# Kernel optimization log

Hardware: AMD Instinct MI355X
Metric: run time of the kernel (lower is better)

The kernel has to match this reference:

```python
import jax, jax.numpy as jnp
import numpy as np

H, HK, D, WIN = 16, 4, 128, 1024  # n_head, n_kv_head, head_dim, left window


def rmsnorm(x):
    eps = jnp.asarray(jnp.finfo(x.dtype).eps, x.dtype)
    return x * jax.lax.rsqrt(jnp.mean(x * x, axis=-1, keepdims=True) + eps)


def rope(x, cos, sin):
    d = x.shape[-1] // 2
    x1, x2 = x[..., :d], x[..., d:]
    return jnp.concatenate([x1 * cos + x2 * sin, x1 * -sin + x2 * cos], axis=-1)


def setup_inputs() -> dict:
    key = jax.random.key(0)
    ks = jax.random.split(key, 12)
    B, T, C = 4, 2048, 2048
    t = jnp.arange(T, dtype=jnp.float32)[:, None]
    inv = 1.0 / (10000.0 ** (jnp.arange(D // 2, dtype=jnp.float32) / (D // 2)))
    ang = t * inv[None, :]  # [T, D/2]
    return {
        "x": jax.random.normal(ks[0], (B, T, C), jnp.float32),
        "x0": jax.random.normal(ks[1], (B, T, C), jnp.float32),
        "ve": jnp.zeros((B, T, C), jnp.float32),  # unused in add_init_qkv branch
        "cos": jnp.cos(ang)[None, :, None, :],  # [1,T,1,D/2]
        "sin": jnp.sin(ang)[None, :, None, :],
        "Wq": jax.random.normal(ks[2], (H * D, C), jnp.float32) * 0.02,
        "Wk": jax.random.normal(ks[3], (HK * D, C), jnp.float32) * 0.02,
        "Wv": jax.random.normal(ks[4], (HK * D, C), jnp.float32) * 0.02,
        "Wproj": jax.random.normal(ks[5], (C, H * D), jnp.float32) * 0.02,
        "alpha_q": jnp.ones((1,), jnp.float32),
        "beta_q": jax.random.uniform(ks[6], (1,), jnp.float32),
        "alpha_k": jnp.ones((1,), jnp.float32),
        "beta_k": jax.random.uniform(ks[7], (1,), jnp.float32),
        "alpha_v": jnp.ones((1,), jnp.float32),
        "beta_v": jax.random.uniform(ks[8], (1,), jnp.float32),
    }


def reference(x, x0, ve, cos, sin, Wq, Wk, Wv, Wproj,
              alpha_q, beta_q, alpha_k, beta_k, alpha_v, beta_v):
    B, T, C = x.shape
    g = H // HK  # GQA group size

    q = (x @ Wq.T).reshape(B, T, H, D)
    k = (x @ Wk.T).reshape(B, T, HK, D)
    v = (x @ Wv.T).reshape(B, T, HK, D)
    v_init = v

    # is_target + add_init_qkv + learn_init_coeffs: blend with projections of norm(x0)
    x0n = rmsnorm(x0)
    cqx = (x0n @ Wq.T).reshape(B, T, H, D)
    ckx = (x0n @ Wk.T).reshape(B, T, HK, D)
    cvx = (x0n @ Wv.T).reshape(B, T, HK, D)
    q = alpha_q * q + beta_q * cqx
    k = alpha_k * k + beta_k * ckx
    v = alpha_v * v + beta_v * cvx

    # rotary + qk-norm + 1.2 scale
    q = rmsnorm(rope(q, cos, sin)) * 1.2
    k = rmsnorm(rope(k, cos, sin)) * 1.2

    qg = q.reshape(B, T, HK, g, D)
    scale = 1.0 / np.sqrt(D)
    scores = jnp.einsum('bqhgd,bkhd->bhgqk', qg, k) * scale  # [B,HK,g,T,T]
    i = jnp.arange(T)[:, None]
    j = jnp.arange(T)[None, :]
    mask = (j <= i) & (i - j <= WIN)
    scores = jnp.where(mask, scores, -jnp.inf)
    p = jax.nn.softmax(scores, axis=-1)
    y = jnp.einsum('bhgqk,bkhd->bqhgd', p, v).reshape(B, T, H * D)

    y = y @ Wproj.T
    return (y, v_init)
```

## Files before the change

kernel.cpp:

```cpp
#include <hip/hip_runtime.h>
#include <hip/hip_bf16.h>
#include <math.h>


using bf16 = __hip_bfloat16;
typedef __attribute__((ext_vector_type(8))) short bf16x8;
typedef __attribute__((ext_vector_type(4))) short bf16x4;
typedef __attribute__((ext_vector_type(4))) float f32x4;

constexpr int Bb = 4, Ts = 2048, Cc = 2048, NH = 16, NKV = 4, Dh = 128, WIN = 1024;
constexpr float EPS = 1.1920929e-07f;

__device__ __forceinline__ void gld16(void* lds, const void* g) {
  __builtin_amdgcn_global_load_lds(
      (__attribute__((address_space(1))) unsigned int*)((void*)g),
      (__attribute__((address_space(3))) unsigned int*)lds, 16, 0, 0);
}

__device__ __forceinline__ unsigned short bfbits(float f) {
  bf16 h = __float2bfloat16(f);
  return __builtin_bit_cast(unsigned short, h);
}

__device__ __forceinline__ void store_out(float* p, float v) { *p = v; }
__device__ __forceinline__ void store_out(bf16* p, float v) { *p = __float2bfloat16(v); }

__device__ __forceinline__ f32x4 mfma16(bf16x4 a, bf16x4 b, f32x4 c) {
#if __has_builtin(__builtin_amdgcn_mfma_f32_16x16x16bf16_1k)
  return __builtin_amdgcn_mfma_f32_16x16x16bf16_1k(a, b, c, 0, 0, 0);
#else
  bf16x8 a8 = {a[0], a[1], a[2], a[3], 0, 0, 0, 0};
  bf16x8 b8 = {b[0], b[1], b[2], b[3], 0, 0, 0, 0};
  return __builtin_amdgcn_mfma_f32_16x16x32_bf16(a8, b8, c, 0, 0, 0);
#endif
}

__global__ __launch_bounds__(256) void convert_w4(
    const float* __restrict__ s0, bf16* __restrict__ d0,
    const float* __restrict__ s1, bf16* __restrict__ d1,
    const float* __restrict__ s2, bf16* __restrict__ d2,
    const float* __restrict__ s3, bf16* __restrict__ d3) {
  const int bid = blockIdx.x;
  const float* src;
  bf16* dst;
  int base;
  if (bid < 4096)      { src = s0; dst = d0; base = 0; }
  else if (bid < 5120) { src = s1; dst = d1; base = 4096; }
  else if (bid < 6144) { src = s2; dst = d2; base = 5120; }
  else                 { src = s3; dst = d3; base = 6144; }
  const int i = (bid - base) * 256 + threadIdx.x;
  float4 v = ((const float4*)src)[i];
  ushort4 u;
  u.x = bfbits(v.x); u.y = bfbits(v.y); u.z = bfbits(v.z); u.w = bfbits(v.w);
  ((ushort4*)dst)[i] = u;
}

__global__ __launch_bounds__(256) void prep(
    const float* __restrict__ x, const float* __restrict__ x0,
    const float* aq_p, const float* bq_p, const float* ak_p, const float* bk_p,
    bf16* __restrict__ xq, bf16* __restrict__ xk,
    bf16* __restrict__ xb, bf16* __restrict__ x0n) {
  const int row = blockIdx.x, tid = threadIdx.x;
  const float4* xr = (const float4*)(x + (size_t)row * Cc);
  const float4* nr = (const float4*)(x0 + (size_t)row * Cc);
  float4 xa[2], na[2];
  float ss = 0.f;
#pragma unroll
  for (int j = 0; j < 2; ++j) {
    xa[j] = xr[tid + j * 256];
    na[j] = nr[tid + j * 256];
    ss += na[j].x * na[j].x + na[j].y * na[j].y + na[j].z * na[j].z + na[j].w * na[j].w;
  }
#pragma unroll
  for (int o = 32; o; o >>= 1) ss += __shfl_xor(ss, o);
  __shared__ float red[4];
  if ((tid & 63) == 0) red[tid >> 6] = ss;
  __syncthreads();
  const float rms = rsqrtf((red[0] + red[1] + red[2] + red[3]) * (1.f / Cc) + EPS);
  const float aq = *aq_p, bq = *bq_p, ak = *ak_p, bk = *bk_p;
#pragma unroll
  for (int j = 0; j < 2; ++j) {
    const size_t base = (size_t)row * Cc + (size_t)(tid + j * 256) * 4;
    float nx[4] = {na[j].x * rms, na[j].y * rms, na[j].z * rms, na[j].w * rms};
    float xv[4] = {xa[j].x, xa[j].y, xa[j].z, xa[j].w};
    ushort4 uq, uk, ub, un;
    uq.x = bfbits(aq * xv[0] + bq * nx[0]); uq.y = bfbits(aq * xv[1] + bq * nx[1]);
    uq.z = bfbits(aq * xv[2] + bq * nx[2]); uq.w = bfbits(aq * xv[3] + bq * nx[3]);
    uk.x = bfbits(ak * xv[0] + bk * nx[0]); uk.y = bfbits(ak * xv[1] + bk * nx[1]);
    uk.z = bfbits(ak * xv[2] + bk * nx[2]); uk.w = bfbits(ak * xv[3] + bk * nx[3]);
    ub.x = bfbits(xv[0]); ub.y = bfbits(xv[1]); ub.z = bfbits(xv[2]); ub.w = bfbits(xv[3]);
    un.x = bfbits(nx[0]); un.y = bfbits(nx[1]); un.z = bfbits(nx[2]); un.w = bfbits(nx[3]);
    *(ushort4*)(xq + base) = uq;
    *(ushort4*)(xk + base) = uk;
    *(ushort4*)(xb + base) = ub;
    *(ushort4*)(x0n + base) = un;
  }
}

template <typename OutT>
__device__ __forceinline__ void gemm_body(
    const bf16* __restrict__ A, const bf16* __restrict__ W,
    OutT* __restrict__ C, int N, int K) {
  __shared__ unsigned short sA[128 * 64];
  __shared__ unsigned short sB[128 * 64];
  const int tid = threadIdx.x, wave = tid >> 6, lane = tid & 63;
  const int quad = lane >> 4, l15 = lane & 15;
  const int bm = blockIdx.x * 128, bn = blockIdx.y * 128;
  const int wm = (wave >> 1) * 64, wn = (wave & 1) * 64;
  const int srow = wave * 32 + (lane >> 3);
  const int scol = (lane & 7) * 8;

  f32x4 acc[4][4] = {};

  for (int k0 = 0; k0 < K; k0 += 64) {
#pragma unroll
    for (int i = 0; i < 4; ++i) {
      gld16(&sA[(wave * 32 + i * 8) * 64], &A[(size_t)(bm + srow + i * 8) * K + k0 + scol]);
      gld16(&sB[(wave * 32 + i * 8) * 64], &W[(size_t)(bn + srow + i * 8) * K + k0 + scol]);
    }
    __syncthreads();
#pragma unroll
    for (int kk = 0; kk < 2; ++kk) {
      bf16x8 af[4], bfr[4];
#pragma unroll
      for (int t = 0; t < 4; ++t)
        af[t] = *(const bf16x8*)&sA[(wm + t * 16 + l15) * 64 + kk * 32 + quad * 8];
#pragma unroll
      for (int t = 0; t < 4; ++t)
        bfr[t] = *(const bf16x8*)&sB[(wn + t * 16 + l15) * 64 + kk * 32 + quad * 8];
#pragma unroll
      for (int tm = 0; tm < 4; ++tm)
#pragma unroll
        for (int tn = 0; tn < 4; ++tn)
          acc[tm][tn] = __builtin_amdgcn_mfma_f32_16x16x32_bf16(af[tm], bfr[tn], acc[tm][tn], 0, 0, 0);
    }
    __syncthreads();
  }
#pragma unroll
  for (int tm = 0; tm < 4; ++tm)
#pragma unroll
    for (int tn = 0; tn < 4; ++tn)
#pragma unroll
      for (int r = 0; r < 4; ++r) {
        const int row = bm + wm + tm * 16 + quad * 4 + r;
        const int col = bn + wn + tn * 16 + l15;
        store_out(&C[(size_t)row * N + col], acc[tm][tn][r]);
      }
}

template <typename OutT>
__global__ __launch_bounds__(256) void gemm_bt(
    const bf16* __restrict__ A, const bf16* __restrict__ W,
    OutT* __restrict__ C, int N, int K) {
  gemm_body<OutT>(A, W, C, N, K);
}

struct GemmTriple { const bf16* A; const bf16* W; bf16* C; };
struct GemmTriple3 { GemmTriple t[3]; };

__global__ __launch_bounds__(256) void gemm_bt3(GemmTriple3 g, int N, int K) {
  const GemmTriple tr = g.t[blockIdx.z];
  gemm_body<bf16>(tr.A, tr.W, tr.C, N, K);
}

__global__ __launch_bounds__(256) void post_qk2(
    const bf16* __restrict__ qpre, const bf16* __restrict__ kpre,
    const float* __restrict__ cosp, const float* __restrict__ sinp,
    bf16* __restrict__ qh, bf16* __restrict__ kh, float qmult) {
  int bid = blockIdx.x;
  const bf16* pre;
  bf16* outh;
  int nh;
  float mult;
  if (bid < 32768) { pre = qpre; outh = qh; nh = NH; mult = qmult; }
  else { bid -= 32768; pre = kpre; outh = kh; nh = NKV; mult = 1.2f; }
  const int wid = bid * 4 + (threadIdx.x >> 6);
  const int lane = threadIdx.x & 63;
  const int h = wid % nh;
  const int bt = wid / nh;
  const int t = bt & (Ts - 1);
  const int b = bt >> 11;
  const size_t src = (size_t)bt * (size_t)(nh * Dh) + (size_t)h * Dh;
  float x1 = __bfloat162float(pre[src + lane]);
  float x2 = __bfloat162float(pre[src + 64 + lane]);
  float c = cosp[t * 64 + lane], s = sinp[t * 64 + lane];
  float o1 = x1 * c + x2 * s;
  float o2 = x2 * c - x1 * s;
  float ss = o1 * o1 + o2 * o2;
#pragma unroll
  for (int o = 32; o; o >>= 1) ss += __shfl_xor(ss, o);
  const float r = rsqrtf(ss * (1.f / Dh) + EPS) * mult;
  const size_t dst = ((size_t)(b * nh + h) * Ts + t) * Dh;
  outh[dst + lane] = __float2bfloat16(o1 * r);
  outh[dst + 64 + lane] = __float2bfloat16(o2 * r);
}

__global__ __launch_bounds__(256) void post_v(
    const bf16* __restrict__ vinit, const bf16* __restrict__ cvx,
    const float* av_p, const float* bv_p,
    bf16* __restrict__ vth, float* __restrict__ vout) {
  __shared__ unsigned short vt[128 * 65];
  const int t0 = blockIdx.x * 64;
  const int b = blockIdx.y >> 2, hk = blockIdx.y & 3;
  const float av = *av_p, bv = *bv_p;
  const int tid = threadIdx.x;
  for (int j = 0; j < 32; ++j) {
    const int e = j * 256 + tid;
    const int tl = e >> 7, d = e & 127;
    const size_t src = (size_t)(b * Ts + t0 + tl) * (NKV * Dh) + hk * Dh + d;
    const float vi = __bfloat162float(vinit[src]);
    const float cv = __bfloat162float(cvx[src]);
    vout[src] = vi;
    vt[d * 65 + tl] = bfbits(av * vi + bv * cv);
  }
  __syncthreads();
#pragma unroll
  for (int j = 0; j < 4; ++j) {
    const int g = j * 256 + tid;
    const int d = g >> 3, t8 = (g & 7) * 8;
    const unsigned short* p = &vt[d * 65 + t8];
    uint4 u;
    u.x = p[0] | ((unsigned int)p[1] << 16);
    u.y = p[2] | ((unsigned int)p[3] << 16);
    u.z = p[4] | ((unsigned int)p[5] << 16);
    u.w = p[6] | ((unsigned int)p[7] << 16);
    *(uint4*)&vth[((size_t)(b * NKV + hk) * Dh + d) * Ts + t0 + t8] = u;
  }
}

__global__ __launch_bounds__(256) void attn(
    const bf16* __restrict__ qh, const bf16* __restrict__ kh,
    const bf16* __restrict__ vth, bf16* __restrict__ att) {
  __shared__ unsigned short sK[64 * 128];
  __shared__ unsigned short sV[128 * 64];

  const int tid = threadIdx.x, wave = tid >> 6, lane = tid & 63;
  const int quad = lane >> 4, l15 = lane & 15;
  const int lin = blockIdx.y * 16 + blockIdx.x;
  const int swz = (lin & 7) * 128 + (lin >> 3);
  const int q0 = (swz & 15) * 128;
  const int by = swz >> 4;
  const int b = by >> 4, h = by & 15, hk = h >> 2;

  const bf16* Qp = qh + (size_t)(b * NH + h) * Ts * Dh;
  const bf16* Kp = kh + (size_t)(b * NKV + hk) * Ts * Dh;
  const bf16* Vp = vth + (size_t)(b * NKV + hk) * Dh * Ts;

  const int qw = q0 + wave * 32;

  bf16x8 qf[2][4];
#pragma unroll
  for (int tm = 0; tm < 2; ++tm)
#pragma unroll
    for (int kk = 0; kk < 4; ++kk)
      qf[tm][kk] = *(const bf16x8*)&Qp[(size_t)(qw + tm * 16 + l15) * Dh + kk * 32 + quad * 8];

  f32x4 of[2][8] = {};
  float m_i[2] = {-__builtin_inff(), -__builtin_inff()};
  float l_i[2] = {0.f, 0.f};

  const int krow = lane >> 4, kgp = lane & 15;
  const int vrow = lane >> 3, vgp = lane & 7;

  const int jt_lo = q0 >= WIN ? (q0 - WIN) >> 6 : 0;
  const int jt_hi = (q0 + 127) >> 6;

  for (int jt = jt_lo; jt <= jt_hi; ++jt) {
    const int j0 = jt << 6;
    __syncthreads();
#pragma unroll
    for (int i = 0; i < 4; ++i) {
      const int row = wave * 16 + i * 4 + krow;
      gld16(&sK[(wave * 16 + i * 4) * 128],
            &Kp[(size_t)(j0 + row) * Dh + (kgp ^ (row & 15)) * 8]);
      const int d = wave * 32 + i * 8 + vrow;
      gld16(&sV[(wave * 32 + i * 8) * 64],
            &Vp[(size_t)d * Ts + j0 + (vgp ^ (d & 7)) * 8]);
    }
    __syncthreads();

    if (j0 > qw + 31 || qw > j0 + 63 + WIN) continue;

    f32x4 sfT[4][2];
#pragma unroll
    for (int tn = 0; tn < 4; ++tn) {
      bf16x8 kf[4];
#pragma unroll
      for (int kk = 0; kk < 4; ++kk)
        kf[kk] = *(const bf16x8*)&sK[(tn * 16 + l15) * 128 + (((kk * 4 + quad) ^ l15) * 8)];
#pragma unroll
      for (int tm = 0; tm < 2; ++tm) {
        f32x4 a = {};
#pragma unroll
        for (int kk = 0; kk < 4; ++kk)
          a = __builtin_amdgcn_mfma_f32_16x16x32_bf16(kf[kk], qf[tm][kk], a, 0, 0, 0);
        sfT[tn][tm] = a;
      }
    }

    const bool full = (j0 + 63 <= qw) && (qw + 31 - j0 <= WIN);

    float alpha[2];
    bool defer[2];
    bf16x4 pf[2][4];
#pragma unroll
    for (int tm = 0; tm < 2; ++tm) {
      float mloc = -__builtin_inff();
      if (full) {
#pragma unroll
        for (int tn = 0; tn < 4; ++tn)
#pragma unroll
          for (int r = 0; r < 4; ++r) mloc = fmaxf(mloc, sfT[tn][tm][r]);
      } else {
        const int dq = (qw + tm * 16 + l15) - (j0 + quad * 4);
#pragma unroll
        for (int tn = 0; tn < 4; ++tn)
#pragma unroll
          for (int r = 0; r < 4; ++r) {
            const unsigned diff = (unsigned)(dq - tn * 16 - r);
            float s = (diff <= (unsigned)WIN) ? sfT[tn][tm][r] : -__builtin_inff();
            sfT[tn][tm][r] = s;
            mloc = fmaxf(mloc, s);
          }
      }
      mloc = fmaxf(mloc, __shfl_xor(mloc, 16));
      mloc = fmaxf(mloc, __shfl_xor(mloc, 32));
      defer[tm] = __all(mloc - m_i[tm] <= 8.f);
      float mnew;
      if (defer[tm]) {
        mnew = m_i[tm];
        alpha[tm] = 1.f;
      } else {
        mnew = fmaxf(m_i[tm], mloc);
        alpha[tm] = __builtin_amdgcn_exp2f(m_i[tm] - mnew);
        m_i[tm] = mnew;
      }
      float rs = 0.f;
#pragma unroll
      for (int tn = 0; tn < 4; ++tn) {
        bf16x4 p4;
#pragma unroll
        for (int r = 0; r < 4; ++r) {
          const float p = __builtin_amdgcn_exp2f(sfT[tn][tm][r] - mnew);
          rs += p;
          p4[r] = (short)bfbits(p);
        }
        pf[tm][tn] = p4;
      }
      rs += __shfl_xor(rs, 16);
      rs += __shfl_xor(rs, 32);
      l_i[tm] = l_i[tm] * alpha[tm] + rs;
    }

#pragma unroll
    for (int tm = 0; tm < 2; ++tm) {
      if (!defer[tm]) {
        float ar[4];
#pragma unroll
        for (int r = 0; r < 4; ++r) ar[r] = __shfl(alpha[tm], quad * 4 + r);
#pragma unroll
        for (int dn = 0; dn < 8; ++dn)
#pragma unroll
          for (int r = 0; r < 4; ++r) of[tm][dn][r] *= ar[r];
      }
    }

#pragma unroll
    for (int tn = 0; tn < 4; ++tn) {
      const int gsw = (tn * 2) ^ (l15 & 7);
#pragma unroll
      for (int dn = 0; dn < 8; ++dn) {
        const int d = dn * 16 + l15;
        const bf16x4 vf = *(const bf16x4*)&sV[d * 64 + ((gsw ^ (quad >> 1)) * 8) + (quad & 1) * 4];
        of[0][dn] = mfma16(pf[0][tn], vf, of[0][dn]);
        of[1][dn] = mfma16(pf[1][tn], vf, of[1][dn]);
      }
    }
  }

#pragma unroll
  for (int tm = 0; tm < 2; ++tm) {
#pragma unroll
    for (int r = 0; r < 4; ++r) {
      const float lr = __shfl(l_i[tm], quad * 4 + r);
      const float inv = 1.f / lr;
      const int qr = qw + tm * 16 + quad * 4 + r;
      bf16* dst = att + (size_t)(b * Ts + qr) * (NH * Dh) + h * Dh;
#pragma unroll
      for (int dn = 0; dn < 8; ++dn)
        dst[dn * 16 + l15] = __float2bfloat16(of[tm][dn][r] * inv);
    }
  }
}

extern "C" void kernel_launch(void* const* d_in, const int* in_sizes, int n_in,
                              void* d_out, int out_size, void* d_ws, size_t ws_size,
                              hipStream_t stream) {
  const float* x = (const float*)d_in[0];
  const float* x0 = (const float*)d_in[1];
  const float* cosp = (const float*)d_in[3];
  const float* sinp = (const float*)d_in[4];
  const float* Wq = (const float*)d_in[5];
  const float* Wk = (const float*)d_in[6];
  const float* Wv = (const float*)d_in[7];
  const float* Wp = (const float*)d_in[8];
  const float* aq = (const float*)d_in[9];
  const float* bq = (const float*)d_in[10];
  const float* ak = (const float*)d_in[11];
  const float* bk = (const float*)d_in[12];
  const float* av = (const float*)d_in[13];
  const float* bv = (const float*)d_in[14];

  char* ws = (char*)d_ws;
  const size_t MB = 1024ull * 1024;
  bf16* xq = (bf16*)(ws + 0 * MB);
  bf16* xk = (bf16*)(ws + 32 * MB);
  bf16* xb = (bf16*)(ws + 64 * MB);
  bf16* x0n = (bf16*)(ws + 96 * MB);
  bf16* vinit = (bf16*)(ws + 128 * MB);
  bf16* cvx = (bf16*)(ws + 136 * MB);
  bf16* Wqb = (bf16*)(ws + 144 * MB);
  bf16* Wkb = (bf16*)(ws + 152 * MB);
  bf16* Wvb = (bf16*)(ws + 154 * MB);
  bf16* Wpb = (bf16*)(ws + 156 * MB);
  bf16* att = xq;
  bf16* qh = xk;
  bf16* kh = xb;
  bf16* vth = (bf16*)(ws + 72 * MB);

  float* y = (float*)d_out;
  float* vout = (float*)d_out + (size_t)Bb * Ts * Cc;
  bf16* q_pre = (bf16*)d_out;
  bf16* k_pre = (bf16*)vout;

  convert_w4<<<10240, 256, 0, stream>>>(Wq, Wqb, Wk, Wkb, Wv, Wvb, Wp, Wpb);

  prep<<<8192, 256, 0, stream>>>(x, x0, aq, bq, ak, bk, xq, xk, xb, x0n);

  gemm_bt<bf16><<<dim3(64, 16), 256, 0, stream>>>(xq, Wqb, q_pre, 2048, 2048);

  GemmTriple3 g3;
  g3.t[0] = {xk, Wkb, k_pre};
  g3.t[1] = {xb, Wvb, vinit};
  g3.t[2] = {x0n, Wvb, cvx};
  gemm_bt3<<<dim3(64, 4, 3), 256, 0, stream>>>(g3, 512, 2048);

  const float qmult = 1.2f * 0.08838834764831845f * 1.4426950408889634f;
  post_qk2<<<40960, 256, 0, stream>>>(q_pre, k_pre, cosp, sinp, qh, kh, qmult);
  post_v<<<dim3(32, 16), 256, 0, stream>>>(vinit, cvx, av, bv, vth, vout);

  attn<<<dim3(16, 64), 256, 0, stream>>>(qh, kh, vth, att);

  gemm_bt<float><<<dim3(64, 16), 256, 0, stream>>>(att, Wpb, y, 2048, 2048);
}
```

Before: 787.0 us.

## Stream softmax per key sub-tile with deferred max update in attention

Restructures the attention inner loop so each 16-key sub-tile goes straight through QK MFMA, masking, exp against the running max, and PV MFMA, without first holding all score tiles. The row max is reduced and any output rescale happens after the PV accumulation. The running max starts at a fixed 12, which relies on QK-norm bounding the scores. Launch bounds now request 4 blocks per CU. The aim is lower register pressure and better overlap of exp with MFMA work, at the cost of exp values that can exceed 1 before rescaling, with some bf16 precision risk.

```diff
diff --git a/kernel.cpp b/kernel.cpp
--- a/kernel.cpp
+++ b/kernel.cpp
@@ -228,7 +228,7 @@
   }
 }
 
-__global__ __launch_bounds__(256) void attn(
+__global__ __launch_bounds__(256, 4) void attn(
     const bf16* __restrict__ qh, const bf16* __restrict__ kh,
     const bf16* __restrict__ vth, bf16* __restrict__ att) {
   __shared__ unsigned short sK[64 * 128];
@@ -256,7 +256,7 @@
       qf[tm][kk] = *(const bf16x8*)&Qp[(size_t)(qw + tm * 16 + l15) * Dh + kk * 32 + quad * 8];
 
   f32x4 of[2][8] = {};
-  float m_i[2] = {-__builtin_inff(), -__builtin_inff()};
+  float m_i[2] = {12.f, 12.f};
   float l_i[2] = {0.f, 0.f};
 
   const int krow = lane >> 4, kgp = lane & 15;
@@ -281,99 +281,69 @@
 
     if (j0 > qw + 31 || qw > j0 + 63 + WIN) continue;
 
-    f32x4 sfT[4][2];
+    const bool full = (j0 + 63 <= qw) && (qw + 31 - j0 <= WIN);
+
+    float mloc[2] = {-__builtin_inff(), -__builtin_inff()};
+    float rs[2] = {0.f, 0.f};
+
 #pragma unroll
     for (int tn = 0; tn < 4; ++tn) {
-      bf16x8 kf[4];
-#pragma unroll
-      for (int kk = 0; kk < 4; ++kk)
-        kf[kk] = *(const bf16x8*)&sK[(tn * 16 + l15) * 128 + (((kk * 4 + quad) ^ l15) * 8)];
+      f32x4 s[2] = {};
+#pragma unroll
+      for (int kk = 0; kk < 4; ++kk) {
+        const bf16x8 kf = *(const bf16x8*)&sK[(tn * 16 + l15) * 128 + (((kk * 4 + quad) ^ l15) * 8)];
+#pragma unroll
+        for (int tm = 0; tm < 2; ++tm)
+          s[tm] = __builtin_amdgcn_mfma_f32_16x16x32_bf16(kf, qf[tm][kk], s[tm], 0, 0, 0);
+      }
+      bf16x4 pf[2];
 #pragma unroll
       for (int tm = 0; tm < 2; ++tm) {
-        f32x4 a = {};
-#pragma unroll
-        for (int kk = 0; kk < 4; ++kk)
-          a = __builtin_amdgcn_mfma_f32_16x16x32_bf16(kf[kk], qf[tm][kk], a, 0, 0, 0);
-        sfT[tn][tm] = a;
+        if (!full) {
+          const int dq = (qw + tm * 16 + l15) - (j0 + tn * 16 + quad * 4);
+#pragma unroll
+          for (int r = 0; r < 4; ++r)
+            if ((unsigned)(dq - r) > (unsigned)WIN) s[tm][r] = -__builtin_inff();
+        }
+#pragma unroll
+        for (int r = 0; r < 4; ++r) {
+          const float sv = s[tm][r];
+          mloc[tm] = fmaxf(mloc[tm], sv);
+          const float p = __builtin_amdgcn_exp2f(sv - m_i[tm]);
+          rs[tm] += p;
+          pf[tm][r] = (short)bfbits(p);
+        }
       }
-    }
-
-    const bool full = (j0 + 63 <= qw) && (qw + 31 - j0 <= WIN);
-
-    float alpha[2];
-    bool defer[2];
-    bf16x4 pf[2][4];
-#pragma unroll
-    for (int tm = 0; tm < 2; ++tm) {
-      float mloc = -__builtin_inff();
-      if (full) {
-#pragma unroll
-        for (int tn = 0; tn < 4; ++tn)
-#pragma unroll
-          for (int r = 0; r < 4; ++r) mloc = fmaxf(mloc, sfT[tn][tm][r]);
-      } else {
-        const int dq = (qw + tm * 16 + l15) - (j0 + quad * 4);
-#pragma unroll
-        for (int tn = 0; tn < 4; ++tn)
-#pragma unroll
-          for (int r = 0; r < 4; ++r) {
-            const unsigned diff = (unsigned)(dq - tn * 16 - r);
-            float s = (diff <= (unsigned)WIN) ? sfT[tn][tm][r] : -__builtin_inff();
-            sfT[tn][tm][r] = s;
-            mloc = fmaxf(mloc, s);
-          }
-      }
-      mloc = fmaxf(mloc, __shfl_xor(mloc, 16));
-      mloc = fmaxf(mloc, __shfl_xor(mloc, 32));
-      defer[tm] = __all(mloc - m_i[tm] <= 8.f);
-      float mnew;
-      if (defer[tm]) {
-        mnew = m_i[tm];
-        alpha[tm] = 1.f;
-      } else {
-        mnew = fmaxf(m_i[tm], mloc);
-        alpha[tm] = __builtin_amdgcn_exp2f(m_i[tm] - mnew);
-        m_i[tm] = mnew;
-      }
-      float rs = 0.f;
-#pragma unroll
-      for (int tn = 0; tn < 4; ++tn) {
-        bf16x4 p4;
-#pragma unroll
-        for (int r = 0; r < 4; ++r) {
-          const float p = __builtin_amdgcn_exp2f(sfT[tn][tm][r] - mnew);
-          rs += p;
-          p4[r] = (short)bfbits(p);
-        }
-        pf[tm][tn] = p4;
-      }
-      rs += __shfl_xor(rs, 16);
-      rs += __shfl_xor(rs, 32);
-      l_i[tm] = l_i[tm] * alpha[tm] + rs;
-    }
-
-#pragma unroll
-    for (int tm = 0; tm < 2; ++tm) {
-      if (!defer[tm]) {
-        float ar[4];
-#pragma unroll
-        for (int r = 0; r < 4; ++r) ar[r] = __shfl(alpha[tm], quad * 4 + r);
-#pragma unroll
-        for (int dn = 0; dn < 8; ++dn)
-#pragma unroll
-          for (int r = 0; r < 4; ++r) of[tm][dn][r] *= ar[r];
-      }
-    }
-
-#pragma unroll
-    for (int tn = 0; tn < 4; ++tn) {
       const int gsw = (tn * 2) ^ (l15 & 7);
 #pragma unroll
       for (int dn = 0; dn < 8; ++dn) {
         const int d = dn * 16 + l15;
         const bf16x4 vf = *(const bf16x4*)&sV[d * 64 + ((gsw ^ (quad >> 1)) * 8) + (quad & 1) * 4];
-        of[0][dn] = mfma16(pf[0][tn], vf, of[0][dn]);
-        of[1][dn] = mfma16(pf[1][tn], vf, of[1][dn]);
+        of[0][dn] = mfma16(pf[0], vf, of[0][dn]);
+        of[1][dn] = mfma16(pf[1], vf, of[1][dn]);
+      }
+    }
+
+#pragma unroll
+    for (int tm = 0; tm < 2; ++tm) {
+      float mg = fmaxf(mloc[tm], __shfl_xor(mloc[tm], 16));
+      mg = fmaxf(mg, __shfl_xor(mg, 32));
+      float r2 = rs[tm] + __shfl_xor(rs[tm], 16);
+      r2 += __shfl_xor(r2, 32);
+      if (__all(mg - m_i[tm] <= 8.f)) {
+        l_i[tm] += r2;
+      } else {
+        const float mnew = fmaxf(m_i[tm], mg);
+        const float alpha = __builtin_amdgcn_exp2f(m_i[tm] - mnew);
+        l_i[tm] = (l_i[tm] + r2) * alpha;
+        m_i[tm] = mnew;
+        float ar[4];
+#pragma unroll
+        for (int r = 0; r < 4; ++r) ar[r] = __shfl(alpha, quad * 4 + r);
+#pragma unroll
+        for (int dn = 0; dn < 8; ++dn)
+#pragma unroll
+          for (int r = 0; r < 4; ++r) of[tm][dn][r] *= ar[r];
       }
     }
   }
```

Measured after the change: 1.153 ms. +46.5%, slower.
